# Kernel tuning notes

Hardware: AMD Instinct MI355X
Metric: run time of the kernel (lower is better)

## Reference

```python
import jax, jax.numpy as jnp
import numpy as np

N_NODES = 100000
N_EDGES = 1600000
NFEAT = 128
NHID = 128
NCLASS = 64


def setup_inputs() -> dict:
    key = jax.random.key(0)
    ks = jax.random.split(key, 8)
    x = jax.random.normal(ks[0], (N_NODES, NFEAT), dtype=jnp.float32)
    edge_src = jax.random.randint(ks[1], (N_EDGES,), 0, N_NODES, dtype=jnp.int32)
    edge_dst = jax.random.randint(ks[2], (N_EDGES,), 0, N_NODES, dtype=jnp.int32)
    edge_w = jax.random.uniform(ks[3], (N_EDGES,), dtype=jnp.float32)
    W0 = jax.random.normal(ks[4], (NFEAT, NHID), dtype=jnp.float32) * (2.0 / (NFEAT + NHID)) ** 0.5
    b0 = jax.random.normal(ks[5], (1, NHID), dtype=jnp.float32) * 0.02
    W1 = jax.random.normal(ks[6], (NHID, NCLASS), dtype=jnp.float32) * (2.0 / (NHID + NCLASS)) ** 0.5
    b1 = jax.random.normal(ks[7], (1, NCLASS), dtype=jnp.float32) * 0.02
    return {"x": x, "edge_src": edge_src, "edge_dst": edge_dst, "edge_w": edge_w,
            "W0": W0, "b0": b0, "W1": W1, "b1": b1}


def _spmm(edge_src, edge_dst, edge_w, h):
    # A_norm @ h via gather + weighted segment-sum over edges. [E,d] gather dominates.
    msgs = h[edge_src] * edge_w[:, None]          # [E, d]
    return jax.ops.segment_sum(msgs, edge_dst, num_segments=N_NODES)  # [N, d]


def reference(x, edge_src, edge_dst, edge_w, W0, b0, W1, b1):
    # Layer 1: aggregate -> linear -> bias -> ReLU (dropout=0, eval mode)
    h = _spmm(edge_src, edge_dst, edge_w, x)      # [N, nfeat]
    h = jax.nn.relu(h @ W0 + b0)                  # [N, nhid]
    # Layer 2 (output layer): aggregate -> linear -> bias
    h = _spmm(edge_src, edge_dst, edge_w, h)      # [N, nhid]
    h = h @ W1 + b1                               # [N, nclass]
    return jax.nn.log_softmax(h, axis=1)
```

## Files before the change

kernel.cpp:

```cpp
#include <hip/hip_runtime.h>

#define NF 128
#define NC 64
#define NBMAX 512
#define TPART 8192
#define BCAP 5120
#define WPITCH 136

static inline size_t alignup(size_t x){ return (x + 255) & ~(size_t)255; }

typedef __attribute__((ext_vector_type(8))) short bf16x8;
typedef __attribute__((ext_vector_type(4))) float f32x4;
typedef __attribute__((ext_vector_type(16))) int i32x16;

__device__ __forceinline__ unsigned short f2bf(float f){
  unsigned u = __float_as_uint(f);
  u += 0x7fffu + ((u >> 16) & 1u);
  return (unsigned short)(u >> 16);
}
__device__ __forceinline__ float bflo(unsigned u){ return __uint_as_float(u << 16); }
__device__ __forceinline__ float bfhi(unsigned u){ return __uint_as_float(u & 0xffff0000u); }

__device__ __forceinline__ void sload16_issue(i32x16& r, const int2* p){
  asm volatile("s_load_dwordx16 %0, %1, 0x0" : "=s"(r) : "s"(p));
}
__device__ __forceinline__ void swait2(i32x16& a, i32x16& b){
  asm volatile("s_waitcnt lgkmcnt(0)" : "+s"(a), "+s"(b));
}
__device__ __forceinline__ void swait4(i32x16& a, i32x16& b, i32x16& c, i32x16& d){
  asm volatile("s_waitcnt lgkmcnt(0)" : "+s"(a), "+s"(b), "+s"(c), "+s"(d));
}

__global__ __launch_bounds__(256) void k_cvtW(const float* __restrict__ W0, const float* __restrict__ W1,
                                              unsigned short* __restrict__ W0t, unsigned short* __restrict__ W1t,
                                              int* __restrict__ bcur, int NB){
  int t = blockIdx.x*256 + threadIdx.x;
  if (t < NB) bcur[t] = t * BCAP;
  if (t < 128*128){ int k = t >> 7, c = t & 127; W0t[c*128 + k] = f2bf(W0[t]); }
  int u = t - 128*128;
  if (u >= 0 && u < 128*64){ int k = u >> 6, c = u & 63; W1t[c*128 + k] = f2bf(W1[u]); }
}

__global__ __launch_bounds__(1024, 4) void k_partg(const int* __restrict__ src, const int* __restrict__ dst,
    const float* __restrict__ w, int* __restrict__ bcur, int2* __restrict__ part, int E, int NB, int PB,
    const float* __restrict__ A, const unsigned short* __restrict__ Wg, unsigned short* __restrict__ Y, int n){
  __shared__ __align__(16) char smem[TPART*8 + NBMAX*16];
  const int t = threadIdx.x;
  if ((int)blockIdx.x < PB){
    int2* stage = (int2*)smem;
    int* hist  = (int*)(smem + TPART*8);
    int* scn   = hist + NBMAX;
    int* cnt2  = scn + NBMAX;
    int* baseg = cnt2 + NBMAX;
    const int t0 = blockIdx.x * TPART;
    if (t < NBMAX){ hist[t] = 0; cnt2[t] = 0; }
    __syncthreads();
    #pragma unroll 4
    for (int k = 0; k < 8; ++k){
      int i = t0 + (k << 10) + t;
      if (i < E) atomicAdd(&hist[dst[i] >> 8], 1);
    }
    __syncthreads();
    if (t < NBMAX) scn[t] = hist[t];
    __syncthreads();
    for (int o = 1; o < NBMAX; o <<= 1){
      int a = (t >= o && t < NBMAX) ? scn[t-o] : 0;
      __syncthreads();
      if (t < NBMAX) scn[t] += a;
      __syncthreads();
    }
    if (t < NB) baseg[t] = hist[t] ? atomicAdd(&bcur[t], hist[t]) : 0;
    __syncthreads();
    #pragma unroll 4
    for (int k = 0; k < 8; ++k){
      int i = t0 + (k << 10) + t;
      if (i < E){
        int d = dst[i], b = d >> 8;
        int r = atomicAdd(&cnt2[b], 1);
        stage[scn[b] - hist[b] + r] = make_int2(((d & 255) << 17) | src[i], __float_as_int(w[i]));
      }
    }
    __syncthreads();
    int wv = t >> 6, ln = t & 63;
    for (int b = wv; b < NB; b += 16){
      int c = hist[b];
      if (!c) continue;
      int lo = scn[b] - c, gb = baseg[b];
      for (int s2 = ln; s2 < c; s2 += 64) part[gb + s2] = stage[lo + s2];
    }
  } else {
    unsigned short* Wt = (unsigned short*)smem;
    for (int i = t; i < 128*16; i += 1024){
      int r = i >> 4, c = (i & 15) << 3;
      *(uint4*)(Wt + r*WPITCH + c) = *(const uint4*)(Wg + r*128 + c);
    }
    __syncthreads();
    const int lane = t & 63, wv = t >> 6;
    const int r0 = (blockIdx.x - PB)*256 + wv*16;
    int rA = r0 + (lane & 15); if (rA > n-1) rA = n-1;
    const int kq = (lane >> 4) << 3;
    f32x4 acc[8] = {};
    #pragma unroll
    for (int kk = 0; kk < 4; ++kk){
      const float* ap = A + (size_t)rA*NF + kk*32 + kq;
      float4 a0 = *(const float4*)ap;
      float4 a1 = *(const float4*)(ap + 4);
      bf16x8 af;
      af[0]=(short)f2bf(a0.x); af[1]=(short)f2bf(a0.y); af[2]=(short)f2bf(a0.z); af[3]=(short)f2bf(a0.w);
      af[4]=(short)f2bf(a1.x); af[5]=(short)f2bf(a1.y); af[6]=(short)f2bf(a1.z); af[7]=(short)f2bf(a1.w);
      const unsigned short* wp = Wt + (lane & 15)*WPITCH + kk*32 + kq;
      #pragma unroll
      for (int nt = 0; nt < 8; ++nt){
        bf16x8 bf = *(const bf16x8*)(wp + nt*16*WPITCH);
        acc[nt] = __builtin_amdgcn_mfma_f32_16x16x32_bf16(af, bf, acc[nt], 0, 0, 0);
      }
    }
    const int rb = r0 + ((lane >> 4) << 2);
    #pragma unroll
    for (int j = 0; j < 4; ++j){
      int rg = rb + j;
      if (rg < n){
        unsigned short* yp = Y + (size_t)rg*NF + (lane & 15);
        #pragma unroll
        for (int nt = 0; nt < 8; ++nt) yp[nt*16] = f2bf(acc[nt][j]);
      }
    }
  }
}

__global__ __launch_bounds__(512) void k_fill2(const int2* __restrict__ part, const int* __restrict__ bcur,
    int2* __restrict__ noff, int2* __restrict__ csr, int N){
  __shared__ int deg[256], scn[256], c2[256];
  const int b = blockIdx.x, t = threadIdx.x;
  const int base = b * BCAP;
  const int cnt = bcur[b] - base;
  const int d0 = b << 8;
  const int nd = min(256, N - d0);
  if (t < 256){ deg[t] = 0; c2[t] = 0; }
  __syncthreads();
  for (int s = t; s < cnt; s += 512) atomicAdd(&deg[(part[base+s].x >> 17) & 255], 1);
  __syncthreads();
  if (t < 256) scn[t] = deg[t];
  __syncthreads();
  for (int o = 1; o < 256; o <<= 1){
    int a = (t < 256 && t >= o) ? scn[t-o] : 0;
    __syncthreads();
    if (t < 256) scn[t] += a;
    __syncthreads();
  }
  if (t < nd) noff[d0 + t] = make_int2(base + scn[t] - deg[t], base + scn[t]);
  __syncthreads();
  for (int s = t; s < cnt; s += 512){
    int2 rec = part[base + s];
    int dl = (rec.x >> 17) & 255;
    int p = base + scn[dl] - deg[dl] + atomicAdd(&c2[dl], 1);
    csr[p] = make_int2(rec.x & 0x1FFFF, rec.y);
  }
}

__global__ __launch_bounds__(256) void k_gemm2(const unsigned short* __restrict__ Ab, const unsigned short* __restrict__ Wg,
                                               unsigned short* __restrict__ G, int n){
  __shared__ unsigned short Wt[64*WPITCH];
  const int tid = threadIdx.x;
  for (int i = tid; i < 64*16; i += 256){
    int r = i >> 4, c = (i & 15) << 3;
    *(uint4*)(Wt + r*WPITCH + c) = *(const uint4*)(Wg + r*128 + c);
  }
  __syncthreads();
  const int lane = tid & 63, wv = tid >> 6;
  const int r0 = blockIdx.x*64 + wv*16;
  int rA = r0 + (lane & 15); if (rA > n-1) rA = n-1;
  const int kq = (lane >> 4) << 3;
  f32x4 acc[4] = {};
  #pragma unroll
  for (int kk = 0; kk < 4; ++kk){
    bf16x8 af = *(const bf16x8*)(Ab + (size_t)rA*NF + kk*32 + kq);
    const unsigned short* wp = Wt + (lane & 15)*WPITCH + kk*32 + kq;
    #pragma unroll
    for (int nt = 0; nt < 4; ++nt){
      bf16x8 bf = *(const bf16x8*)(wp + nt*16*WPITCH);
      acc[nt] = __builtin_amdgcn_mfma_f32_16x16x32_bf16(af, bf, acc[nt], 0, 0, 0);
    }
  }
  const int rb = r0 + ((lane >> 4) << 2);
  #pragma unroll
  for (int j = 0; j < 4; ++j){
    int rg = rb + j;
    if (rg < n){
      unsigned short* gp = G + (size_t)rg*NC + (lane & 15);
      #pragma unroll
      for (int nt = 0; nt < 4; ++nt) gp[nt*16] = f2bf(acc[nt][j]);
    }
  }
}

__global__ __launch_bounds__(256, 6) void k_spmm_relu(const unsigned short* __restrict__ y, const int2* __restrict__ csr,
    const int2* __restrict__ noff, const float* __restrict__ bias, unsigned short* __restrict__ h, int n){
  int wid  = (blockIdx.x * 256 + threadIdx.x) >> 6;
  int lane = threadIdx.x & 63;
  if (wid >= n) return;
  const int2 se = noff[wid];
  const int s = __builtin_amdgcn_readfirstlane(se.x);
  const int e = __builtin_amdgcn_readfirstlane(se.y);
  const int half = lane >> 5, li = lane & 31;
  const unsigned liOff = (unsigned)li << 3;
  const char* yb = (const char*)y;
  float a0x[2]={0.f,0.f}, a0y[2]={0.f,0.f}, a1x[2]={0.f,0.f}, a1y[2]={0.f,0.f};
  const int deg = e - s;

#define RELU_FMA(VV, WW)                                                      \
    _Pragma("unroll")                                                         \
    for (int k = 0; k < 8; ++k){                                              \
      a0x[k&1] = fmaf(WW[k], bflo(VV[k].x), a0x[k&1]);                        \
      a0y[k&1] = fmaf(WW[k], bfhi(VV[k].x), a0y[k&1]);                        \
      a1x[k&1] = fmaf(WW[k], bflo(VV[k].y), a1x[k&1]);                        \
      a1y[k&1] = fmaf(WW[k], bfhi(VV[k].y), a1y[k&1]);                        \
    }

  if (deg > 0 && deg <= 16){
    i32x16 rA, rB;
    sload16_issue(rA, csr + s);
    sload16_issue(rB, csr + s + 8);
    swait2(rA, rB);
    const int jbh = s + (half << 3);
    unsigned offk[8]; float wk[8];
    #pragma unroll
    for (int k = 0; k < 8; ++k){
      int r  = half ? rB[2*k]   : rA[2*k];
      int wb = half ? rB[2*k+1] : rA[2*k+1];
      r = ((unsigned)r < (unsigned)n) ? r : 0;
      offk[k] = ((unsigned)r << 8) + liOff;
      wk[k] = (jbh + k < e) ? __int_as_float(wb) : 0.f;
    }
    uint2 v[8];
    #pragma unroll
    for (int k = 0; k < 8; ++k) v[k] = *(const uint2*)(yb + offk[k]);
    __builtin_amdgcn_sched_barrier(0);
    RELU_FMA(v, wk)
  } else if (deg > 16 && deg <= 32){
    i32x16 rA0, rB0, rA1, rB1;
    sload16_issue(rA0, csr + s);
    sload16_issue(rB0, csr + s + 8);
    sload16_issue(rA1, csr + e - 16);
    sload16_issue(rB1, csr + e - 8);
    swait4(rA0, rB0, rA1, rB1);
    const int lo1 = s + 16;
    const int t1 = (e - 16) + (half << 3);
    unsigned off0[8], off1[8]; float wk0[8], wk1[8];
    #pragma unroll
    for (int k = 0; k < 8; ++k){
      int r0v = half ? rB0[2*k] : rA0[2*k];
      int w0v = half ? rB0[2*k+1] : rA0[2*k+1];
      off0[k] = ((unsigned)r0v << 8) + liOff;
      wk0[k] = __int_as_float(w0v);
      int r1v = half ? rB1[2*k] : rA1[2*k];
      int w1v = half ? rB1[2*k+1] : rA1[2*k+1];
      off1[k] = ((unsigned)r1v << 8) + liOff;
      wk1[k] = (t1 + k >= lo1) ? __int_as_float(w1v) : 0.f;
    }
    uint2 v0[8], v1[8];
    #pragma unroll
    for (int k = 0; k < 8; ++k) v0[k] = *(const uint2*)(yb + off0[k]);
    #pragma unroll
    for (int k = 0; k < 8; ++k) v1[k] = *(const uint2*)(yb + off1[k]);
    __builtin_amdgcn_sched_barrier(0);
    RELU_FMA(v0, wk0)
    RELU_FMA(v1, wk1)
  } else if (deg > 32){
    int jb = s;
    const int nfull = deg >> 4;
    for (int b = 0; b < nfull; ++b, jb += 16){
      i32x16 rA, rB;
      sload16_issue(rA, csr + jb);
      sload16_issue(rB, csr + jb + 8);
      swait2(rA, rB);
      unsigned offk[8]; float wk[8];
      #pragma unroll
      for (int k = 0; k < 8; ++k){
        int r  = half ? rB[2*k]   : rA[2*k];
        int wb = half ? rB[2*k+1] : rA[2*k+1];
        offk[k] = ((unsigned)r << 8) + liOff;
        wk[k] = __int_as_float(wb);
      }
      uint2 v[8];
      #pragma unroll
      for (int k = 0; k < 8; ++k) v[k] = *(const uint2*)(yb + offk[k]);
      __builtin_amdgcn_sched_barrier(0);
      RELU_FMA(v, wk)
    }
    if (jb < e){
      i32x16 rA, rB;
      sload16_issue(rA, csr + e - 16);
      sload16_issue(rB, csr + e - 8);
      swait2(rA, rB);
      const int t1 = (e - 16) + (half << 3);
      unsigned offk[8]; float wk[8];
      #pragma unroll
      for (int k = 0; k < 8; ++k){
        int r  = half ? rB[2*k]   : rA[2*k];
        int wb = half ? rB[2*k+1] : rA[2*k+1];
        offk[k] = ((unsigned)r << 8) + liOff;
        wk[k] = (t1 + k >= jb) ? __int_as_float(wb) : 0.f;
      }
      uint2 v[8];
      #pragma unroll
      for (int k = 0; k < 8; ++k) v[k] = *(const uint2*)(yb + offk[k]);
      __builtin_amdgcn_sched_barrier(0);
      RELU_FMA(v, wk)
    }
  }
#undef RELU_FMA
  float o0 = a0x[0]+a0x[1], o1 = a0y[0]+a0y[1], o2 = a1x[0]+a1x[1], o3 = a1y[0]+a1y[1];
  o0 += __shfl_xor(o0, 32); o1 += __shfl_xor(o1, 32);
  o2 += __shfl_xor(o2, 32); o3 += __shfl_xor(o3, 32);
  float4 bb = ((const float4*)bias)[li];
  o0 = fmaxf(o0 + bb.x, 0.f); o1 = fmaxf(o1 + bb.y, 0.f);
  o2 = fmaxf(o2 + bb.z, 0.f); o3 = fmaxf(o3 + bb.w, 0.f);
  if (half == 0){
    uint2 p;
    p.x = (unsigned)f2bf(o0) | ((unsigned)f2bf(o1) << 16);
    p.y = (unsigned)f2bf(o2) | ((unsigned)f2bf(o3) << 16);
    *(uint2*)(h + (size_t)wid * NF + li*4) = p;
  }
}

__global__ __launch_bounds__(256, 6) void k_spmm_ls(const unsigned short* __restrict__ g, const int2* __restrict__ csr,
    const int2* __restrict__ noff, const float* __restrict__ bias, float* __restrict__ out, int n){
  int wid  = (blockIdx.x * 256 + threadIdx.x) >> 6;
  int lane = threadIdx.x & 63;
  if (wid >= n) return;
  const int2 se = noff[wid];
  const int s = __builtin_amdgcn_readfirstlane(se.x);
  const int e = __builtin_amdgcn_readfirstlane(se.y);
  const int half = lane >> 5, li = lane & 31;
  const unsigned liOff = (unsigned)li << 2;
  const char* gb = (const char*)g;
  float z0[2]={0.f,0.f}, z1[2]={0.f,0.f};
  const int deg = e - s;

#define LS_FMA(VV, WW)                                                        \
    _Pragma("unroll")                                                         \
    for (int k = 0; k < 8; ++k){                                              \
      z0[k&1] = fmaf(WW[k], bflo(VV[k]), z0[k&1]);                            \
      z1[k&1] = fmaf(WW[k], bfhi(VV[k]), z1[k&1]);                            \
    }

  if (deg > 0 && deg <= 16){
    i32x16 rA, rB;
    sload16_issue(rA, csr + s);
    sload16_issue(rB, csr + s + 8);
    swait2(rA, rB);
    const int jbh = s + (half << 3);
    unsigned offk[8]; float wk[8];
    #pragma unroll
    for (int k = 0; k < 8; ++k){
      int r  = half ? rB[2*k]   : rA[2*k];
      int wb = half ? rB[2*k+1] : rA[2*k+1];
      r = ((unsigned)r < (unsigned)n) ? r : 0;
      offk[k] = ((unsigned)r << 7) + liOff;
      wk[k] = (jbh + k < e) ? __int_as_float(wb) : 0.f;
    }
    unsigned v[8];
    #pragma unroll
    for (int k = 0; k < 8; ++k) v[k] = *(const unsigned*)(gb + offk[k]);
    __builtin_amdgcn_sched_barrier(0);
    LS_FMA(v, wk)
  } else if (deg > 16 && deg <= 32){
    i32x16 rA0, rB0, rA1, rB1;
    sload16_issue(rA0, csr + s);
    sload16_issue(rB0, csr + s + 8);
    sload16_issue(rA1, csr + e - 16);
    sload16_issue(rB1, csr + e - 8);
    swait4(rA0, rB0, rA1, rB1);
    const int lo1 = s + 16;
    const int t1 = (e - 16) + (half << 3);
    unsigned off0[8], off1[8]; float wk0[8], wk1[8];
    #pragma unroll
    for (int k = 0; k < 8; ++k){
      int r0v = half ? rB0[2*k] : rA0[2*k];
      int w0v = half ? rB0[2*k+1] : rA0[2*k+1];
      off0[k] = ((unsigned)r0v << 7) + liOff;
      wk0[k] = __int_as_float(w0v);
      int r1v = half ? rB1[2*k] : rA1[2*k];
      int w1v = half ? rB1[2*k+1] : rA1[2*k+1];
      off1[k] = ((unsigned)r1v << 7) + liOff;
      wk1[k] = (t1 + k >= lo1) ? __int_as_float(w1v) : 0.f;
    }
    unsigned v0[8], v1[8];
    #pragma unroll
    for (int k = 0; k < 8; ++k) v0[k] = *(const unsigned*)(gb + off0[k]);
    #pragma unroll
    for (int k = 0; k < 8; ++k) v1[k] = *(const unsigned*)(gb + off1[k]);
    __builtin_amdgcn_sched_barrier(0);
    LS_FMA(v0, wk0)
    LS_FMA(v1, wk1)
  } else if (deg > 32){
    int jb = s;
    const int nfull = deg >> 4;
    for (int b = 0; b < nfull; ++b, jb += 16){
      i32x16 rA, rB;
      sload16_issue(rA, csr + jb);
      sload16_issue(rB, csr + jb + 8);
      swait2(rA, rB);
      unsigned offk[8]; float wk[8];
      #pragma unroll
      for (int k = 0; k < 8; ++k){
        int r  = half ? rB[2*k]   : rA[2*k];
        int wb = half ? rB[2*k+1] : rA[2*k+1];
        offk[k] = ((unsigned)r << 7) + liOff;
        wk[k] = __int_as_float(wb);
      }
      unsigned v[8];
      #pragma unroll
      for (int k = 0; k < 8; ++k) v[k] = *(const unsigned*)(gb + offk[k]);
      __builtin_amdgcn_sched_barrier(0);
      LS_FMA(v, wk)
    }
    if (jb < e){
      i32x16 rA, rB;
      sload16_issue(rA, csr + e - 16);
      sload16_issue(rB, csr + e - 8);
      swait2(rA, rB);
      const int t1 = (e - 16) + (half << 3);
      unsigned offk[8]; float wk[8];
      #pragma unroll
      for (int k = 0; k < 8; ++k){
        int r  = half ? rB[2*k]   : rA[2*k];
        int wb = half ? rB[2*k+1] : rA[2*k+1];
        offk[k] = ((unsigned)r << 7) + liOff;
        wk[k] = (t1 + k >= jb) ? __int_as_float(wb) : 0.f;
      }
      unsigned v[8];
      #pragma unroll
      for (int k = 0; k < 8; ++k) v[k] = *(const unsigned*)(gb + offk[k]);
      __builtin_amdgcn_sched_barrier(0);
      LS_FMA(v, wk)
    }
  }
#undef LS_FMA
  float zz0 = z0[0]+z0[1], zz1 = z1[0]+z1[1];
  zz0 += __shfl_xor(zz0, 32); zz1 += __shfl_xor(zz1, 32);
  float2 bb = ((const float2*)bias)[li];
  zz0 += bb.x; zz1 += bb.y;
  float m = fmaxf(zz0, zz1);
  for (int o = 16; o; o >>= 1) m = fmaxf(m, __shfl_xor(m, o));
  float sum = expf(zz0 - m) + expf(zz1 - m);
  for (int o = 16; o; o >>= 1) sum += __shfl_xor(sum, o);
  float lg = logf(sum);
  if (half == 0)
    *(float2*)(out + (size_t)wid * NC + li*2) = make_float2(zz0 - m - lg, zz1 - m - lg);
}

extern "C" void kernel_launch(void* const* d_in, const int* in_sizes, int n_in,
                              void* d_out, int out_size, void* d_ws, size_t ws_size,
                              hipStream_t stream){
  const float* x  = (const float*)d_in[0];
  const int* esrc = (const int*)d_in[1];
  const int* edst = (const int*)d_in[2];
  const float* ew = (const float*)d_in[3];
  const float* W0 = (const float*)d_in[4];
  const float* b0 = (const float*)d_in[5];
  const float* W1 = (const float*)d_in[6];
  const float* b1 = (const float*)d_in[7];
  float* out = (float*)d_out;

  const int N = in_sizes[0] / NF;
  const int E = in_sizes[1];
  const int NB = (N + 255) >> 8;

  char* ws = (char*)d_ws;
  size_t o = 0;
  int*  bcur  = (int*) (ws + o); o = alignup(o + NBMAX*4);
  int2* noff  = (int2*)(ws + o); o = alignup(o + (size_t)N*8);
  unsigned short* W0t = (unsigned short*)(ws + o); o = alignup(o + 128*128*2);
  unsigned short* W1t = (unsigned short*)(ws + o); o = alignup(o + 128*64*2);
  int2* part  = (int2*)(ws + o); o = alignup(o + (size_t)NB*BCAP*8);
  int2* csr   = (int2*)(ws + o); o = alignup(o + (size_t)NB*BCAP*8 + 256);
  unsigned short* y  = (unsigned short*)(ws + o); o = alignup(o + (size_t)N*NF*2);
  unsigned short* hb = (unsigned short*)(ws + o); o = alignup(o + (size_t)N*NF*2);
  unsigned short* g = y;

  const int pb  = (E + TPART-1)/TPART;
  const int gb1 = (N + 255)/256;

  k_cvtW <<<96, 256, 0, stream>>>(W0, W1, W0t, W1t, bcur, NB);
  k_partg<<<pb + gb1, 1024, 0, stream>>>(esrc, edst, ew, bcur, part, E, NB, pb,
                                         x, W0t, y, N);
  k_fill2<<<NB, 512, 0, stream>>>(part, bcur, noff, csr, N);

  const int gb = (N + 63)/64;
  const int sb = (N + 3)/4;

  k_spmm_relu<<<sb, 256, 0, stream>>>(y, csr, noff, b0, hb, N);
  k_gemm2<<<gb, 256, 0, stream>>>(hb, W1t, g, N);
  k_spmm_ls<<<sb, 256, 0, stream>>>(g, csr, noff, b1, out, N);
}
```

Baseline: 167.7 us.

## Fuse first-layer SpMM+ReLU with second GEMM via shared-memory tile

Merges the layer-1 aggregation kernel and the hidden-to-class GEMM into one 1024-thread kernel. Each of the block's 16 waves aggregates one node into a shared-memory tile, then wave 0 runs MFMA on that 16-row tile and writes the 64-wide output. This removes the global write and re-read of the bf16 hidden matrix and one kernel launch. In exchange, blocks are much larger, there is a block-wide barrier, and the GEMM runs on one wave while the other 15 sit idle at the end of each block. Imbalanced node degrees within a block can also stall the whole block.

```diff
diff --git a/kernel.cpp b/kernel.cpp
--- a/kernel.cpp
+++ b/kernel.cpp
@@ -158,55 +158,27 @@
   }
 }
 
-__global__ __launch_bounds__(256) void k_gemm2(const unsigned short* __restrict__ Ab, const unsigned short* __restrict__ Wg,
-                                               unsigned short* __restrict__ G, int n){
+__global__ __launch_bounds__(1024, 2) void k_spmm_g2(const unsigned short* __restrict__ y, const int2* __restrict__ csr,
+    const int2* __restrict__ noff, const float* __restrict__ bias, const unsigned short* __restrict__ Wg,
+    unsigned short* __restrict__ G, int n){
   __shared__ unsigned short Wt[64*WPITCH];
-  const int tid = threadIdx.x;
-  for (int i = tid; i < 64*16; i += 256){
+  __shared__ unsigned short hbS[16*WPITCH];
+  const int t = threadIdx.x;
+  for (int i = t; i < 64*16; i += 1024){
     int r = i >> 4, c = (i & 15) << 3;
     *(uint4*)(Wt + r*WPITCH + c) = *(const uint4*)(Wg + r*128 + c);
   }
-  __syncthreads();
-  const int lane = tid & 63, wv = tid >> 6;
-  const int r0 = blockIdx.x*64 + wv*16;
-  int rA = r0 + (lane & 15); if (rA > n-1) rA = n-1;
-  const int kq = (lane >> 4) << 3;
-  f32x4 acc[4] = {};
-  #pragma unroll
-  for (int kk = 0; kk < 4; ++kk){
-    bf16x8 af = *(const bf16x8*)(Ab + (size_t)rA*NF + kk*32 + kq);
-    const unsigned short* wp = Wt + (lane & 15)*WPITCH + kk*32 + kq;
-    #pragma unroll
-    for (int nt = 0; nt < 4; ++nt){
-      bf16x8 bf = *(const bf16x8*)(wp + nt*16*WPITCH);
-      acc[nt] = __builtin_amdgcn_mfma_f32_16x16x32_bf16(af, bf, acc[nt], 0, 0, 0);
-    }
-  }
-  const int rb = r0 + ((lane >> 4) << 2);
-  #pragma unroll
-  for (int j = 0; j < 4; ++j){
-    int rg = rb + j;
-    if (rg < n){
-      unsigned short* gp = G + (size_t)rg*NC + (lane & 15);
-      #pragma unroll
-      for (int nt = 0; nt < 4; ++nt) gp[nt*16] = f2bf(acc[nt][j]);
-    }
-  }
-}
-
-__global__ __launch_bounds__(256, 6) void k_spmm_relu(const unsigned short* __restrict__ y, const int2* __restrict__ csr,
-    const int2* __restrict__ noff, const float* __restrict__ bias, unsigned short* __restrict__ h, int n){
-  int wid  = (blockIdx.x * 256 + threadIdx.x) >> 6;
-  int lane = threadIdx.x & 63;
-  if (wid >= n) return;
-  const int2 se = noff[wid];
-  const int s = __builtin_amdgcn_readfirstlane(se.x);
-  const int e = __builtin_amdgcn_readfirstlane(se.y);
+  const int wv = t >> 6, lane = t & 63;
+  const int wid = blockIdx.x*16 + wv;
   const int half = lane >> 5, li = lane & 31;
-  const unsigned liOff = (unsigned)li << 3;
-  const char* yb = (const char*)y;
-  float a0x[2]={0.f,0.f}, a0y[2]={0.f,0.f}, a1x[2]={0.f,0.f}, a1y[2]={0.f,0.f};
-  const int deg = e - s;
+  if (wid < n){
+    const int2 se = noff[wid];
+    const int s = __builtin_amdgcn_readfirstlane(se.x);
+    const int e = __builtin_amdgcn_readfirstlane(se.y);
+    const unsigned liOff = (unsigned)li << 3;
+    const char* yb = (const char*)y;
+    float a0x[2]={0.f,0.f}, a0y[2]={0.f,0.f}, a1x[2]={0.f,0.f}, a1y[2]={0.f,0.f};
+    const int deg = e - s;
 
 #define RELU_FMA(VV, WW)                                                      \
     _Pragma("unroll")                                                         \
@@ -217,110 +189,136 @@
       a1y[k&1] = fmaf(WW[k], bfhi(VV[k].y), a1y[k&1]);                        \
     }
 
-  if (deg > 0 && deg <= 16){
-    i32x16 rA, rB;
-    sload16_issue(rA, csr + s);
-    sload16_issue(rB, csr + s + 8);
-    swait2(rA, rB);
-    const int jbh = s + (half << 3);
-    unsigned offk[8]; float wk[8];
-    #pragma unroll
-    for (int k = 0; k < 8; ++k){
-      int r  = half ? rB[2*k]   : rA[2*k];
-      int wb = half ? rB[2*k+1] : rA[2*k+1];
-      r = ((unsigned)r < (unsigned)n) ? r : 0;
-      offk[k] = ((unsigned)r << 8) + liOff;
-      wk[k] = (jbh + k < e) ? __int_as_float(wb) : 0.f;
-    }
-    uint2 v[8];
-    #pragma unroll
-    for (int k = 0; k < 8; ++k) v[k] = *(const uint2*)(yb + offk[k]);
-    __builtin_amdgcn_sched_barrier(0);
-    RELU_FMA(v, wk)
-  } else if (deg > 16 && deg <= 32){
-    i32x16 rA0, rB0, rA1, rB1;
-    sload16_issue(rA0, csr + s);
-    sload16_issue(rB0, csr + s + 8);
-    sload16_issue(rA1, csr + e - 16);
-    sload16_issue(rB1, csr + e - 8);
-    swait4(rA0, rB0, rA1, rB1);
-    const int lo1 = s + 16;
-    const int t1 = (e - 16) + (half << 3);
-    unsigned off0[8], off1[8]; float wk0[8], wk1[8];
-    #pragma unroll
-    for (int k = 0; k < 8; ++k){
-      int r0v = half ? rB0[2*k] : rA0[2*k];
-      int w0v = half ? rB0[2*k+1] : rA0[2*k+1];
-      off0[k] = ((unsigned)r0v << 8) + liOff;
-      wk0[k] = __int_as_float(w0v);
-      int r1v = half ? rB1[2*k] : rA1[2*k];
-      int w1v = half ? rB1[2*k+1] : rA1[2*k+1];
-      off1[k] = ((unsigned)r1v << 8) + liOff;
-      wk1[k] = (t1 + k >= lo1) ? __int_as_float(w1v) : 0.f;
-    }
-    uint2 v0[8], v1[8];
-    #pragma unroll
-    for (int k = 0; k < 8; ++k) v0[k] = *(const uint2*)(yb + off0[k]);
-    #pragma unroll
-    for (int k = 0; k < 8; ++k) v1[k] = *(const uint2*)(yb + off1[k]);
-    __builtin_amdgcn_sched_barrier(0);
-    RELU_FMA(v0, wk0)
-    RELU_FMA(v1, wk1)
-  } else if (deg > 32){
-    int jb = s;
-    const int nfull = deg >> 4;
-    for (int b = 0; b < nfull; ++b, jb += 16){
+    if (deg > 0 && deg <= 16){
       i32x16 rA, rB;
-      sload16_issue(rA, csr + jb);
-      sload16_issue(rB, csr + jb + 8);
+      sload16_issue(rA, csr + s);
+      sload16_issue(rB, csr + s + 8);
       swait2(rA, rB);
+      const int jbh = s + (half << 3);
       unsigned offk[8]; float wk[8];
       #pragma unroll
       for (int k = 0; k < 8; ++k){
         int r  = half ? rB[2*k]   : rA[2*k];
         int wb = half ? rB[2*k+1] : rA[2*k+1];
+        r = ((unsigned)r < (unsigned)n) ? r : 0;
         offk[k] = ((unsigned)r << 8) + liOff;
-        wk[k] = __int_as_float(wb);
+        wk[k] = (jbh + k < e) ? __int_as_float(wb) : 0.f;
       }
       uint2 v[8];
       #pragma unroll
       for (int k = 0; k < 8; ++k) v[k] = *(const uint2*)(yb + offk[k]);
       __builtin_amdgcn_sched_barrier(0);
       RELU_FMA(v, wk)
-    }
-    if (jb < e){
-      i32x16 rA, rB;
-      sload16_issue(rA, csr + e - 16);
-      sload16_issue(rB, csr + e - 8);
-      swait2(rA, rB);
+    } else if (deg > 16 && deg <= 32){
+      i32x16 rA0, rB0, rA1, rB1;
+      sload16_issue(rA0, csr + s);
+      sload16_issue(rB0, csr + s + 8);
+      sload16_issue(rA1, csr + e - 16);
+      sload16_issue(rB1, csr + e - 8);
+      swait4(rA0, rB0, rA1, rB1);
+      const int lo1 = s + 16;
       const int t1 = (e - 16) + (half << 3);
-      unsigned offk[8]; float wk[8];
+      unsigned off0[8], off1[8]; float wk0[8], wk1[8];
       #pragma unroll
       for (int k = 0; k < 8; ++k){
-        int r  = half ? rB[2*k]   : rA[2*k];
-        int wb = half ? rB[2*k+1] : rA[2*k+1];
-        offk[k] = ((unsigned)r << 8) + liOff;
-        wk[k] = (t1 + k >= jb) ? __int_as_float(wb) : 0.f;
-      }
-      uint2 v[8];
-      #pragma unroll
-      for (int k = 0; k < 8; ++k) v[k] = *(const uint2*)(yb + offk[k]);
+        int r0v = half ? rB0[2*k] : rA0[2*k];
+        int w0v = half ? rB0[2*k+1] : rA0[2*k+1];
+        off0[k] = ((unsigned)r0v << 8) + liOff;
+        wk0[k] = __int_as_float(w0v);
+        int r1v = half ? rB1[2*k] : rA1[2*k];
+        int w1v = half ? rB1[2*k+1] : rA1[2*k+1];
+        off1[k] = ((unsigned)r1v << 8) + liOff;
+        wk1[k] = (t1 + k >= lo1) ? __int_as_float(w1v) : 0.f;
+      }
+      uint2 v0[8], v1[8];
+      #pragma unroll
+      for (int k = 0; k < 8; ++k) v0[k] = *(const uint2*)(yb + off0[k]);
+      #pragma unroll
+      for (int k = 0; k < 8; ++k) v1[k] = *(const uint2*)(yb + off1[k]);
       __builtin_amdgcn_sched_barrier(0);
-      RELU_FMA(v, wk)
-    }
-  }
+      RELU_FMA(v0, wk0)
+      RELU_FMA(v1, wk1)
+    } else if (deg > 32){
+      int jb = s;
+      const int nfull = deg >> 4;
+      for (int b = 0; b < nfull; ++b, jb += 16){
+        i32x16 rA, rB;
+        sload16_issue(rA, csr + jb);
+        sload16_issue(rB, csr + jb + 8);
+        swait2(rA, rB);
+        unsigned offk[8]; float wk[8];
+        #pragma unroll
+        for (int k = 0; k < 8; ++k){
+          int r  = half ? rB[2*k]   : rA[2*k];
+          int wb = half ? rB[2*k+1] : rA[2*k+1];
+          offk[k] = ((unsigned)r << 8) + liOff;
+          wk[k] = __int_as_float(wb);
+        }
+        uint2 v[8];
+        #pragma unroll
+        for (int k = 0; k < 8; ++k) v[k] = *(const uint2*)(yb + offk[k]);
+        __builtin_amdgcn_sched_barrier(0);
+        RELU_FMA(v, wk)
+      }
+      if (jb < e){
+        i32x16 rA, rB;
+        sload16_issue(rA, csr + e - 16);
+        sload16_issue(rB, csr + e - 8);
+        swait2(rA, rB);
+        const int t1 = (e - 16) + (half << 3);
+        unsigned offk[8]; float wk[8];
+        #pragma unroll
+        for (int k = 0; k < 8; ++k){
+          int r  = half ? rB[2*k]   : rA[2*k];
+          int wb = half ? rB[2*k+1] : rA[2*k+1];
+          offk[k] = ((unsigned)r << 8) + liOff;
+          wk[k] = (t1 + k >= jb) ? __int_as_float(wb) : 0.f;
+        }
+        uint2 v[8];
+        #pragma unroll
+        for (int k = 0; k < 8; ++k) v[k] = *(const uint2*)(yb + offk[k]);
+        __builtin_amdgcn_sched_barrier(0);
+        RELU_FMA(v, wk)
+      }
+    }
 #undef RELU_FMA
-  float o0 = a0x[0]+a0x[1], o1 = a0y[0]+a0y[1], o2 = a1x[0]+a1x[1], o3 = a1y[0]+a1y[1];
-  o0 += __shfl_xor(o0, 32); o1 += __shfl_xor(o1, 32);
-  o2 += __shfl_xor(o2, 32); o3 += __shfl_xor(o3, 32);
-  float4 bb = ((const float4*)bias)[li];
-  o0 = fmaxf(o0 + bb.x, 0.f); o1 = fmaxf(o1 + bb.y, 0.f);
-  o2 = fmaxf(o2 + bb.z, 0.f); o3 = fmaxf(o3 + bb.w, 0.f);
-  if (half == 0){
-    uint2 p;
-    p.x = (unsigned)f2bf(o0) | ((unsigned)f2bf(o1) << 16);
-    p.y = (unsigned)f2bf(o2) | ((unsigned)f2bf(o3) << 16);
-    *(uint2*)(h + (size_t)wid * NF + li*4) = p;
+    float o0 = a0x[0]+a0x[1], o1 = a0y[0]+a0y[1], o2 = a1x[0]+a1x[1], o3 = a1y[0]+a1y[1];
+    o0 += __shfl_xor(o0, 32); o1 += __shfl_xor(o1, 32);
+    o2 += __shfl_xor(o2, 32); o3 += __shfl_xor(o3, 32);
+    float4 bb = ((const float4*)bias)[li];
+    o0 = fmaxf(o0 + bb.x, 0.f); o1 = fmaxf(o1 + bb.y, 0.f);
+    o2 = fmaxf(o2 + bb.z, 0.f); o3 = fmaxf(o3 + bb.w, 0.f);
+    if (half == 0){
+      uint2 p;
+      p.x = (unsigned)f2bf(o0) | ((unsigned)f2bf(o1) << 16);
+      p.y = (unsigned)f2bf(o2) | ((unsigned)f2bf(o3) << 16);
+      *(uint2*)(hbS + wv*WPITCH + li*4) = p;
+    }
+  }
+  __syncthreads();
+  if (wv == 0){
+    const int kq = (lane >> 4) << 3;
+    f32x4 acc[4] = {};
+    #pragma unroll
+    for (int kk = 0; kk < 4; ++kk){
+      bf16x8 af = *(const bf16x8*)(hbS + (lane & 15)*WPITCH + kk*32 + kq);
+      const unsigned short* wp = Wt + (lane & 15)*WPITCH + kk*32 + kq;
+      #pragma unroll
+      for (int nt = 0; nt < 4; ++nt){
+        bf16x8 bf = *(const bf16x8*)(wp + nt*16*WPITCH);
+        acc[nt] = __builtin_amdgcn_mfma_f32_16x16x32_bf16(af, bf, acc[nt], 0, 0, 0);
+      }
+    }
+    const int rb = (lane >> 4) << 2;
+    #pragma unroll
+    for (int j = 0; j < 4; ++j){
+      int rg = blockIdx.x*16 + rb + j;
+      if (rg < n){
+        unsigned short* gp = G + (size_t)rg*NC + (lane & 15);
+        #pragma unroll
+        for (int nt = 0; nt < 4; ++nt) gp[nt*16] = f2bf(acc[nt][j]);
+      }
+    }
   }
 }
 
@@ -476,9 +474,8 @@
   unsigned short* W1t = (unsigned short*)(ws + o); o = alignup(o + 128*64*2);
   int2* part  = (int2*)(ws + o); o = alignup(o + (size_t)NB*BCAP*8);
   int2* csr   = (int2*)(ws + o); o = alignup(o + (size_t)NB*BCAP*8 + 256);
-  unsigned short* y  = (unsigned short*)(ws + o); o = alignup(o + (size_t)N*NF*2);
-  unsigned short* hb = (unsigned short*)(ws + o); o = alignup(o + (size_t)N*NF*2);
-  unsigned short* g = y;
+  unsigned short* y = (unsigned short*)(ws + o); o = alignup(o + (size_t)N*NF*2);
+  unsigned short* g = (unsigned short*)(ws + o); o = alignup(o + (size_t)N*NC*2);
 
   const int pb  = (E + TPART-1)/TPART;
   const int gb1 = (N + 255)/256;
@@ -488,10 +485,9 @@
                                          x, W0t, y, N);
   k_fill2<<<NB, 512, 0, stream>>>(part, bcur, noff, csr, N);
 
-  const int gb = (N + 63)/64;
+  const int sg = (N + 15)/16;
   const int sb = (N + 3)/4;
 
-  k_spmm_relu<<<sb, 256, 0, stream>>>(y, csr, noff, b0, hb, N);
-  k_gemm2<<<gb, 256, 0, stream>>>(hb, W1t, g, N);
+  k_spmm_g2<<<sg, 1024, 0, stream>>>(y, csr, noff, b0, W1t, g, N);
   k_spmm_ls<<<sb, 256, 0, stream>>>(g, csr, noff, b1, out, N);
 }
```

After: 178.7 us. 1.07x slower.
